# Optimization experiments

Measured on AMD Instinct MI355X. Metric: run time of the kernel, lower is better.

The kernel has to match this reference:

```python
import jax, jax.numpy as jnp
import numpy as np

W0_SIREN = 30.0  # omega_0 used in sine activations

HID = [64, 64, 256, 256, 256]
IN_DIM = 65   # 64 feat channels + 1 time channel
OUT_DIM = 64


def _siren_params(key):
    dims = [IN_DIM] + HID + [OUT_DIM]
    params = []
    for i in range(len(dims) - 1):
        fan_in, fan_out = dims[i], dims[i + 1]
        key, kw, kb = jax.random.split(key, 3)
        if i == 0:
            bound = 1.0 / fan_in
        else:
            bound = np.sqrt(6.0 / fan_in) / W0_SIREN
        W = jax.random.uniform(kw, (fan_out, fan_in), jnp.float32, -bound, bound)
        b = jax.random.uniform(kb, (fan_out,), jnp.float32, -bound, bound)
        params.append((W, b))
    return params


def setup_inputs() -> dict:
    key = jax.random.key(0)
    k_feat, k_t, k_p = jax.random.split(key, 3)
    feat = jax.random.normal(k_feat, (2, 64, 192, 320), jnp.float32)
    times = jax.random.uniform(k_t, (3,), jnp.float32)
    params = _siren_params(k_p)
    inp = {"feat": feat, "times": times}
    for i, (W, b) in enumerate(params):
        inp[f"w{i}"] = W
        inp[f"b{i}"] = b
    return inp


def _gather_full_grid(feat):
    """Nearest grid_sample (align_corners=False) at pixel-center coords over the full grid.
    Returns [B, H*W, C]."""
    B, C, H, W = feat.shape
    # make_coord pixel centers in [-1, 1]
    ys = -1.0 + (2.0 * jnp.arange(H, dtype=jnp.float32) + 1.0) / H
    xs = -1.0 + (2.0 * jnp.arange(W, dtype=jnp.float32) + 1.0) / W
    gy, gx = jnp.meshgrid(ys, xs, indexing="ij")          # [H, W] each
    gy, gx = gy.reshape(-1), gx.reshape(-1)               # [qs]
    # grid_sample nearest, align_corners=False unnormalization
    iy = jnp.clip(jnp.round(((gy + 1.0) * H - 1.0) / 2.0).astype(jnp.int32), 0, H - 1)
    ix = jnp.clip(jnp.round(((gx + 1.0) * W - 1.0) / 2.0).astype(jnp.int32), 0, W - 1)
    q = feat[:, :, iy, ix]                                # [B, C, qs] gather
    return jnp.transpose(q, (0, 2, 1))                    # [B, qs, C]


def _siren_mlp(x, ws, bs):
    h = x
    n = len(ws)
    for i in range(n - 1):
        h = jnp.sin(W0_SIREN * (h @ ws[i].T + bs[i]))
    return h @ ws[n - 1].T + bs[n - 1]                    # outermost linear


def reference(feat, times, w0, b0, w1, b1, w2, b2, w3, b3, w4, b4, w5, b5):
    ws = [w0, w1, w2, w3, w4, w5]
    bs = [b0, b1, b2, b3, b4, b5]
    B, C, H, W = feat.shape
    qs = H * W
    q_feat = _gather_full_grid(feat)                      # [B, qs, 64]
    preds = []
    for c in range(3):  # Training==True branch: 3 time stamps
        t = times[c]
        pe = jnp.full((B, qs, 1), 1.0, feat.dtype) * t    # time channel
        enc = jnp.concatenate([q_feat, pe], axis=-1)      # [B, qs, 65]
        out = _siren_mlp(enc.reshape(B * qs, IN_DIM), ws, bs)  # [B*qs, 64]
        # F.fold with kernel_size=1 == reshape back to spatial map
        pred = out.reshape(B, qs, OUT_DIM).transpose(0, 2, 1).reshape(B, OUT_DIM, H, W)
        preds.append(pred)
    return jnp.stack(preds, axis=0)                       # [3, B, 64, H, W]
```

## Files before the change

### kernel.cpp

```cpp
#include <hip/hip_runtime.h>
#include <hip/hip_bf16.h>

typedef __bf16 bf16_t;
typedef bf16_t bf16x8 __attribute__((ext_vector_type(8)));
typedef float f32x4 __attribute__((ext_vector_type(4)));
typedef unsigned short u16;
typedef unsigned int u32;

static constexpr int kHW = 192 * 320;
static constexpr float kC = 4.77464829275686f;

__device__ __forceinline__ u16 f2bf(float f) {
  u32 u = __float_as_uint(f);
  return (u16)((u + 0x7FFFu + ((u >> 16) & 1u)) >> 16);
}

__device__ __forceinline__ u32 pack2(float a, float b) {
  __hip_bfloat162 h = __float22bfloat162_rn(make_float2(a, b));
  union { __hip_bfloat162 h2; u32 u; } cv;
  cv.h2 = h;
  return cv.u;
}

__device__ __forceinline__ void lds_barrier() {
  __asm__ volatile("s_waitcnt lgkmcnt(0)\n\ts_barrier" ::: "memory");
}

static constexpr int OFF_W0 = 0;
static constexpr int OFF_W1 = 4096;
static constexpr int OFF_W2 = 8192;
static constexpr int OFF_W3 = 24576;
static constexpr int OFF_W4 = 90112;
static constexpr int OFF_W5 = 155648;
static constexpr int W_TOTAL = 172032;
static constexpr int B_TOTAL = 1024;
static constexpr size_t FEAT_BYTE_OFF = 348160;
static constexpr size_t WS_NEED = FEAT_BYTE_OFF + (size_t)1920 * 8192;

__global__ void convert_weights(const float* __restrict__ w0, const float* __restrict__ w1,
                                const float* __restrict__ w2, const float* __restrict__ w3,
                                const float* __restrict__ w4, const float* __restrict__ w5,
                                const float* __restrict__ b0, const float* __restrict__ b1,
                                const float* __restrict__ b2, const float* __restrict__ b3,
                                const float* __restrict__ b4, const float* __restrict__ b5,
                                u16* __restrict__ wb, float* __restrict__ bws) {
  int i = blockIdx.x * 256 + threadIdx.x;
  if (i < W_TOTAL) {
    float v, s = kC;
    if (i < OFF_W1)      { int o = i >> 6, k = i & 63; v = w0[o * 65 + k]; }
    else if (i < OFF_W2) { v = w1[i - OFF_W1]; }
    else if (i < OFF_W3) { v = w2[i - OFF_W2]; }
    else if (i < OFF_W4) { v = w3[i - OFF_W3]; }
    else if (i < OFF_W5) { v = w4[i - OFF_W4]; }
    else                 { v = w5[i - OFF_W5]; s = 1.0f; }
    wb[i] = f2bf(v * s);
  } else {
    int j = i - W_TOTAL;
    float v;
    if (j < 64)       v = kC * b0[j];
    else if (j < 128) v = kC * w0[(j - 64) * 65 + 64];
    else if (j < 192) v = kC * b1[j - 128];
    else if (j < 448) v = kC * b2[j - 192];
    else if (j < 704) v = kC * b3[j - 448];
    else if (j < 960) v = kC * b4[j - 704];
    else              v = b5[j - 960];
    bws[j] = v;
  }
}

__global__ void convert_feat(const float* __restrict__ feat, u16* __restrict__ featT) {
  const int chunk = blockIdx.x;
  const int bq  = chunk / 960;
  const int hw0 = (chunk % 960) * 64;
  const int tid = threadIdx.x;
  const int p   = tid & 63;
  const int gg  = tid >> 6;
  const float* fbase = feat + (size_t)bq * 64 * kHW + hw0 + p;
  u16* img = featT + (size_t)chunk * 4096;
#pragma unroll
  for (int j = 0; j < 2; ++j) {
    const int g = gg * 2 + j;
    float v[8];
#pragma unroll
    for (int e = 0; e < 8; ++e) v[e] = fbase[(size_t)(g * 8 + e) * kHW];
    uint4 pk;
    pk.x = pack2(v[0], v[1]);
    pk.y = pack2(v[2], v[3]);
    pk.z = pack2(v[4], v[5]);
    pk.w = pack2(v[6], v[7]);
    *reinterpret_cast<uint4*>(img + p * 64 + ((g ^ (p & 7)) * 8)) = pk;
  }
}

template<int RSO>
__device__ __forceinline__ void epilogue_sin(f32x4 acc, u16* outb, int p, int g,
                                             int quad, int sw) {
  float s0 = __builtin_amdgcn_sinf(__builtin_amdgcn_fractf(acc[0]));
  float s1 = __builtin_amdgcn_sinf(__builtin_amdgcn_fractf(acc[1]));
  float s2 = __builtin_amdgcn_sinf(__builtin_amdgcn_fractf(acc[2]));
  float s3 = __builtin_amdgcn_sinf(__builtin_amdgcn_fractf(acc[3]));
  uint2 v;
  v.x = pack2(s0, s1);
  v.y = pack2(s2, s3);
  *reinterpret_cast<uint2*>(outb + p * RSO + ((g ^ sw) * 8) + (quad & 1) * 4) = v;
}

__device__ __forceinline__ f32x4 mf(bf16x8 a, bf16x8 b, f32x4 c) {
  return __builtin_amdgcn_mfma_f32_16x16x32_bf16(a, b, c, 0, 0, 0);
}

template<bool PRE>
__global__ __attribute__((amdgpu_waves_per_eu(2, 2)))
void __launch_bounds__(256)
siren_main(const float* __restrict__ feat, const float* __restrict__ times,
           const u16* __restrict__ wb, const float* __restrict__ bws,
           const u16* __restrict__ featT, float* __restrict__ out) {
  __shared__ __align__(16) u16 A32[64 * 256];
  __shared__ __align__(16) u16 B32[64 * 256];
  u16* X = B32;
  u16* Y = B32 + 4096;

  const int tid   = threadIdx.x;
  const int bid   = blockIdx.x;
  const int c     = bid / 1920;
  const int chunk = bid % 1920;
  const int bq    = chunk / 960;
  const int hw0   = (chunk % 960) * 64;
  const float t   = times[c];
  const int wave  = tid >> 6;
  const int lane  = tid & 63;
  const int l15   = lane & 15;
  const int quad  = lane >> 4;
  const int sw    = l15 & 7;

  auto read_af8 = [&](bf16x8 (&af)[8], const u16* in, int pt) {
#pragma unroll
    for (int ks = 0; ks < 8; ++ks)
      af[ks] = *reinterpret_cast<const bf16x8*>(
          in + (pt * 16 + l15) * 256 + (((ks * 4 + quad) ^ sw) * 8));
  };
  auto read_af2 = [&](bf16x8 (&af)[2], const u16* in, int pt) {
#pragma unroll
    for (int ks = 0; ks < 2; ++ks)
      af[ks] = *reinterpret_cast<const bf16x8*>(
          in + (pt * 16 + l15) * 64 + (((ks * 4 + quad) ^ sw) * 8));
  };
  auto load_wf_half = [&](bf16x8 (&wf)[4][4], const u16* wbase, int kh) {
#pragma unroll
    for (int ks = 0; ks < 4; ++ks)
#pragma unroll
      for (int ot = 0; ot < 4; ++ot)
        wf[ot][ks] = *reinterpret_cast<const bf16x8*>(
            wbase + ((wave * 4 + ot) * 16 + l15) * 256 + (kh * 4 + ks) * 32 + quad * 8);
  };
  auto load_bv4 = [&](f32x4 (&bv)[4], const float* bg) {
#pragma unroll
    for (int ot = 0; ot < 4; ++ot)
      bv[ot] = *reinterpret_cast<const f32x4*>(bg + (wave * 4 + ot) * 16 + quad * 4);
  };
  auto mfma_pair = [&](f32x4 (&accA)[4], f32x4 (&accB)[4],
                       bf16x8 (&wa)[4][4], bf16x8 (&wbh)[4][4],
                       bf16x8 (&afA)[8], bf16x8 (&afB)[8], const f32x4 (&bv)[4]) {
#pragma unroll
    for (int ot = 0; ot < 4; ++ot) { accA[ot] = bv[ot]; accB[ot] = bv[ot]; }
#pragma unroll
    for (int ks = 0; ks < 8; ++ks)
#pragma unroll
      for (int ot = 0; ot < 4; ++ot) {
        bf16x8 w = ks < 4 ? wa[ot][ks] : wbh[ot][ks - 4];
        accA[ot] = mf(w, afA[ks], accA[ot]);
        accB[ot] = mf(w, afB[ks], accB[ot]);
      }
  };
  auto epi_pt4 = [&](f32x4 (&acc)[4], u16* outb, int pt) {
#pragma unroll
    for (int ot = 0; ot < 4; ++ot)
      epilogue_sin<256>(acc[ot], outb, pt * 16 + l15,
                        (wave * 4 + ot) * 2 + (quad >> 1), quad, sw);
  };

  bf16x8 wf0[2], wf1[2];
#pragma unroll
  for (int ks = 0; ks < 2; ++ks) {
    wf0[ks] = *reinterpret_cast<const bf16x8*>(wb + OFF_W0 + (wave * 16 + l15) * 64 + ks * 32 + quad * 8);
    wf1[ks] = *reinterpret_cast<const bf16x8*>(wb + OFF_W1 + (wave * 16 + l15) * 64 + ks * 32 + quad * 8);
  }
  f32x4 bv0, bv1;
  {
    f32x4 cb = *reinterpret_cast<const f32x4*>(bws + wave * 16 + quad * 4);
    f32x4 cw = *reinterpret_cast<const f32x4*>(bws + 64 + wave * 16 + quad * 4);
#pragma unroll
    for (int r = 0; r < 4; ++r) bv0[r] = cb[r] + t * cw[r];
    bv1 = *reinterpret_cast<const f32x4*>(bws + 128 + wave * 16 + quad * 4);
  }

  bf16x8 wf2[4][2];
  f32x4  bv2[4];

  if constexpr (PRE) {
    const u16* fsrc = featT + (size_t)chunk * 4096;
    bf16x8 a[4][2];
#pragma unroll
    for (int p = 0; p < 4; ++p)
#pragma unroll
      for (int ks = 0; ks < 2; ++ks)
        a[p][ks] = *reinterpret_cast<const bf16x8*>(
            fsrc + (p * 16 + l15) * 64 + (((ks * 4 + quad) ^ sw) * 8));
#pragma unroll
    for (int ks = 0; ks < 2; ++ks)
#pragma unroll
      for (int ot = 0; ot < 4; ++ot)
        wf2[ot][ks] = *reinterpret_cast<const bf16x8*>(
            wb + OFF_W2 + ((wave * 4 + ot) * 16 + l15) * 64 + ks * 32 + quad * 8);
    load_bv4(bv2, bws + 192);

    f32x4 accp[4];
#pragma unroll
    for (int p = 0; p < 4; ++p) accp[p] = bv0;
#pragma unroll
    for (int ks = 0; ks < 2; ++ks)
#pragma unroll
      for (int p = 0; p < 4; ++p) accp[p] = mf(wf0[ks], a[p][ks], accp[p]);
#pragma unroll
    for (int p = 0; p < 4; ++p)
      epilogue_sin<64>(accp[p], Y, p * 16 + l15, wave * 2 + (quad >> 1), quad, sw);
  } else {
    {
      const int p  = tid & 63;
      const int gg = tid >> 6;
      const float* fbase = feat + (size_t)bq * 64 * kHW + hw0 + p;
#pragma unroll
      for (int j = 0; j < 2; ++j) {
        const int g = gg * 2 + j;
        float v[8];
#pragma unroll
        for (int e = 0; e < 8; ++e) v[e] = fbase[(size_t)(g * 8 + e) * kHW];
        uint4 pk;
        pk.x = pack2(v[0], v[1]);
        pk.y = pack2(v[2], v[3]);
        pk.z = pack2(v[4], v[5]);
        pk.w = pack2(v[6], v[7]);
        *reinterpret_cast<uint4*>(X + p * 64 + ((g ^ (p & 7)) * 8)) = pk;
      }
    }
    lds_barrier();
#pragma unroll
    for (int ks = 0; ks < 2; ++ks)
#pragma unroll
      for (int ot = 0; ot < 4; ++ot)
        wf2[ot][ks] = *reinterpret_cast<const bf16x8*>(
            wb + OFF_W2 + ((wave * 4 + ot) * 16 + l15) * 64 + ks * 32 + quad * 8);
    load_bv4(bv2, bws + 192);
#pragma unroll
    for (int pt = 0; pt < 4; ++pt) {
      bf16x8 a[2];
      read_af2(a, X, pt);
      f32x4 acc = bv0;
      acc = mf(wf0[0], a[0], acc); acc = mf(wf0[1], a[1], acc);
      epilogue_sin<64>(acc, Y, pt * 16 + l15, wave * 2 + (quad >> 1), quad, sw);
    }
  }
  lds_barrier();

  bf16x8 wf3a[4][4], wf3b[4][4];
  f32x4  bv3[4];
  {
    bf16x8 a[4][2];
    read_af2(a[0], Y, 0);
    read_af2(a[1], Y, 1);
    read_af2(a[2], Y, 2);
    read_af2(a[3], Y, 3);
    load_wf_half(wf3a, wb + OFF_W3, 0);
    load_bv4(bv3, bws + 448);
    f32x4 accp[4];
#pragma unroll
    for (int p = 0; p < 4; ++p) accp[p] = bv1;
#pragma unroll
    for (int ks = 0; ks < 2; ++ks)
#pragma unroll
      for (int p = 0; p < 4; ++p) accp[p] = mf(wf1[ks], a[p][ks], accp[p]);
#pragma unroll
    for (int p = 0; p < 4; ++p)
      epilogue_sin<64>(accp[p], X, p * 16 + l15, wave * 2 + (quad >> 1), quad, sw);
  }
  lds_barrier();

  {
    bf16x8 aA[2], aB[2];
    read_af2(aA, X, 0);
    read_af2(aB, X, 1);
    f32x4 accA[4], accB[4];
#pragma unroll
    for (int ot = 0; ot < 4; ++ot) { accA[ot] = bv2[ot]; accB[ot] = bv2[ot]; }
#pragma unroll
    for (int ks = 0; ks < 2; ++ks)
#pragma unroll
      for (int ot = 0; ot < 4; ++ot) {
        accA[ot] = mf(wf2[ot][ks], aA[ks], accA[ot]);
        accB[ot] = mf(wf2[ot][ks], aB[ks], accB[ot]);
      }
    read_af2(aA, X, 2);
    read_af2(aB, X, 3);
    epi_pt4(accA, A32, 0);
    epi_pt4(accB, A32, 1);
#pragma unroll
    for (int ot = 0; ot < 4; ++ot) { accA[ot] = bv2[ot]; accB[ot] = bv2[ot]; }
#pragma unroll
    for (int ks = 0; ks < 2; ++ks)
#pragma unroll
      for (int ot = 0; ot < 4; ++ot) {
        accA[ot] = mf(wf2[ot][ks], aA[ks], accA[ot]);
        accB[ot] = mf(wf2[ot][ks], aB[ks], accB[ot]);
      }
    load_wf_half(wf3b, wb + OFF_W3, 1);
    epi_pt4(accA, A32, 2);
    epi_pt4(accB, A32, 3);
  }
  lds_barrier();

  bf16x8 wf4a[4][4], wf4b[4][4];
  f32x4  bv4[4];
  {
    bf16x8 afA[8], afB[8];
    read_af8(afA, A32, 0);
    read_af8(afB, A32, 1);
    f32x4 accA[4], accB[4];
    mfma_pair(accA, accB, wf3a, wf3b, afA, afB, bv3);
    read_af8(afA, A32, 2);
    read_af8(afB, A32, 3);
    epi_pt4(accA, B32, 0);
    epi_pt4(accB, B32, 1);
    mfma_pair(accA, accB, wf3a, wf3b, afA, afB, bv3);
    load_wf_half(wf4a, wb + OFF_W4, 0);
    load_bv4(bv4, bws + 704);
    epi_pt4(accA, B32, 2);
    epi_pt4(accB, B32, 3);
  }
  lds_barrier();

  bf16x8 wf5[8];
  f32x4  bv5;
  {
    load_wf_half(wf4b, wb + OFF_W4, 1);
    bf16x8 afA[8], afB[8];
    read_af8(afA, B32, 0);
    read_af8(afB, B32, 1);
    f32x4 accA[4], accB[4];
    mfma_pair(accA, accB, wf4a, wf4b, afA, afB, bv4);
    read_af8(afA, B32, 2);
    read_af8(afB, B32, 3);
    epi_pt4(accA, A32, 0);
    epi_pt4(accB, A32, 1);
    mfma_pair(accA, accB, wf4a, wf4b, afA, afB, bv4);
#pragma unroll
    for (int ks = 0; ks < 8; ++ks)
      wf5[ks] = *reinterpret_cast<const bf16x8*>(
          wb + OFF_W5 + (wave * 16 + l15) * 256 + ks * 32 + quad * 8);
    bv5 = *reinterpret_cast<const f32x4*>(bws + 960 + wave * 16 + quad * 4);
    epi_pt4(accA, A32, 2);
    epi_pt4(accB, A32, 3);
  }
  lds_barrier();

  {
    float* out_base = out + (size_t)(c * 2 + bq) * 64 * kHW + hw0;
    const int o = wave * 16 + quad * 4;
    bf16x8 afA[8], afB[8];
    read_af8(afA, A32, 0);
    read_af8(afB, A32, 1);
#pragma unroll
    for (int pp = 0; pp < 2; ++pp) {
      f32x4 accA = bv5, accB = bv5;
#pragma unroll
      for (int ks = 0; ks < 8; ++ks) {
        accA = mf(wf5[ks], afA[ks], accA);
        accB = mf(wf5[ks], afB[ks], accB);
      }
      if (pp == 0) { read_af8(afA, A32, 2); read_af8(afB, A32, 3); }
      const int ptA = pp * 2, ptB = pp * 2 + 1;
      float* dstA = out_base + (size_t)o * kHW + (ptA * 16 + l15);
      float* dstB = out_base + (size_t)o * kHW + (ptB * 16 + l15);
#pragma unroll
      for (int r = 0; r < 4; ++r) dstA[(size_t)r * kHW] = accA[r];
#pragma unroll
      for (int r = 0; r < 4; ++r) dstB[(size_t)r * kHW] = accB[r];
    }
  }
}

extern "C" void kernel_launch(void* const* d_in, const int* in_sizes, int n_in,
                              void* d_out, int out_size, void* d_ws, size_t ws_size,
                              hipStream_t stream) {
  const float* feat  = (const float*)d_in[0];
  const float* times = (const float*)d_in[1];
  const float* w0 = (const float*)d_in[2];
  const float* b0 = (const float*)d_in[3];
  const float* w1 = (const float*)d_in[4];
  const float* b1 = (const float*)d_in[5];
  const float* w2 = (const float*)d_in[6];
  const float* b2 = (const float*)d_in[7];
  const float* w3 = (const float*)d_in[8];
  const float* b3 = (const float*)d_in[9];
  const float* w4 = (const float*)d_in[10];
  const float* b4 = (const float*)d_in[11];
  const float* w5 = (const float*)d_in[12];
  const float* b5 = (const float*)d_in[13];
  u16*   wb  = (u16*)d_ws;
  float* bws = (float*)((char*)d_ws + (size_t)W_TOTAL * 2);
  float* out = (float*)d_out;

  convert_weights<<<(W_TOTAL + B_TOTAL) / 256, 256, 0, stream>>>(
      w0, w1, w2, w3, w4, w5, b0, b1, b2, b3, b4, b5, wb, bws);

  if (ws_size >= WS_NEED) {
    u16* featT = (u16*)((char*)d_ws + FEAT_BYTE_OFF);
    convert_feat<<<1920, 256, 0, stream>>>(feat, featT);
    siren_main<true><<<5760, 256, 0, stream>>>(feat, times, wb, bws, featT, out);
  } else {
    siren_main<false><<<5760, 256, 0, stream>>>(feat, times, wb, bws, wb, out);
  }
}
```

Measured before the change: 386.5 us.

## Double block to 128 points with 8 waves, halving per-wave weight tiles

Each block now handles 128 query points with 512 threads (8 waves) instead of 64 points with 256 threads. In the 256-wide layers each wave owns 32 output channels instead of 64, so the full weight tile for one layer fits in registers at once. The small layers are split by point halves across the two wave groups. The aim is to cut weight-fragment register pressure and amortise weight loads over more points per block. In exchange the block uses twice the LDS (128 KB total), barriers span more waves, and occupancy per CU may change.

```diff
diff --git a/kernel.cpp b/kernel.cpp
--- a/kernel.cpp
+++ b/kernel.cpp
@@ -111,27 +111,29 @@
 
 template<bool PRE>
 __global__ __attribute__((amdgpu_waves_per_eu(2, 2)))
-void __launch_bounds__(256)
+void __launch_bounds__(512)
 siren_main(const float* __restrict__ feat, const float* __restrict__ times,
            const u16* __restrict__ wb, const float* __restrict__ bws,
            const u16* __restrict__ featT, float* __restrict__ out) {
-  __shared__ __align__(16) u16 A32[64 * 256];
-  __shared__ __align__(16) u16 B32[64 * 256];
+  __shared__ __align__(16) u16 A32[128 * 256];
+  __shared__ __align__(16) u16 B32[128 * 256];
   u16* X = B32;
-  u16* Y = B32 + 4096;
+  u16* Y = B32 + 8192;
 
   const int tid   = threadIdx.x;
   const int bid   = blockIdx.x;
-  const int c     = bid / 1920;
-  const int chunk = bid % 1920;
-  const int bq    = chunk / 960;
-  const int hw0   = (chunk % 960) * 64;
+  const int c     = bid / 960;
+  const int pair  = bid % 960;
+  const int bq    = pair / 480;
+  const int hw0   = (pair % 480) * 128;
   const float t   = times[c];
   const int wave  = tid >> 6;
   const int lane  = tid & 63;
   const int l15   = lane & 15;
   const int quad  = lane >> 4;
   const int sw    = l15 & 7;
+  const int wlo   = wave & 3;
+  const int p0    = (wave >> 2) * 4;
 
   auto read_af8 = [&](bf16x8 (&af)[8], const u16* in, int pt) {
 #pragma unroll
@@ -145,89 +147,87 @@
       af[ks] = *reinterpret_cast<const bf16x8*>(
           in + (pt * 16 + l15) * 64 + (((ks * 4 + quad) ^ sw) * 8));
   };
-  auto load_wf_half = [&](bf16x8 (&wf)[4][4], const u16* wbase, int kh) {
-#pragma unroll
-    for (int ks = 0; ks < 4; ++ks)
-#pragma unroll
-      for (int ot = 0; ot < 4; ++ot)
+  auto load_wf16 = [&](bf16x8 (&wf)[2][8], const u16* wbase) {
+#pragma unroll
+    for (int ot = 0; ot < 2; ++ot)
+#pragma unroll
+      for (int ks = 0; ks < 8; ++ks)
         wf[ot][ks] = *reinterpret_cast<const bf16x8*>(
-            wbase + ((wave * 4 + ot) * 16 + l15) * 256 + (kh * 4 + ks) * 32 + quad * 8);
-  };
-  auto load_bv4 = [&](f32x4 (&bv)[4], const float* bg) {
-#pragma unroll
-    for (int ot = 0; ot < 4; ++ot)
-      bv[ot] = *reinterpret_cast<const f32x4*>(bg + (wave * 4 + ot) * 16 + quad * 4);
-  };
-  auto mfma_pair = [&](f32x4 (&accA)[4], f32x4 (&accB)[4],
-                       bf16x8 (&wa)[4][4], bf16x8 (&wbh)[4][4],
-                       bf16x8 (&afA)[8], bf16x8 (&afB)[8], const f32x4 (&bv)[4]) {
-#pragma unroll
-    for (int ot = 0; ot < 4; ++ot) { accA[ot] = bv[ot]; accB[ot] = bv[ot]; }
+            wbase + ((wave * 2 + ot) * 16 + l15) * 256 + ks * 32 + quad * 8);
+  };
+  auto load_bv2 = [&](f32x4 (&bv)[2], const float* bg) {
+#pragma unroll
+    for (int ot = 0; ot < 2; ++ot)
+      bv[ot] = *reinterpret_cast<const f32x4*>(bg + (wave * 2 + ot) * 16 + quad * 4);
+  };
+  auto mfma_pair2 = [&](f32x4 (&accA)[2], f32x4 (&accB)[2], bf16x8 (&wf)[2][8],
+                        bf16x8 (&afA)[8], bf16x8 (&afB)[8], const f32x4 (&bv)[2]) {
+#pragma unroll
+    for (int ot = 0; ot < 2; ++ot) { accA[ot] = bv[ot]; accB[ot] = bv[ot]; }
 #pragma unroll
     for (int ks = 0; ks < 8; ++ks)
 #pragma unroll
-      for (int ot = 0; ot < 4; ++ot) {
-        bf16x8 w = ks < 4 ? wa[ot][ks] : wbh[ot][ks - 4];
-        accA[ot] = mf(w, afA[ks], accA[ot]);
-        accB[ot] = mf(w, afB[ks], accB[ot]);
+      for (int ot = 0; ot < 2; ++ot) {
+        accA[ot] = mf(wf[ot][ks], afA[ks], accA[ot]);
+        accB[ot] = mf(wf[ot][ks], afB[ks], accB[ot]);
       }
   };
-  auto epi_pt4 = [&](f32x4 (&acc)[4], u16* outb, int pt) {
-#pragma unroll
-    for (int ot = 0; ot < 4; ++ot)
+  auto epi_pt2 = [&](f32x4 (&acc)[2], u16* outb, int pt) {
+#pragma unroll
+    for (int ot = 0; ot < 2; ++ot)
       epilogue_sin<256>(acc[ot], outb, pt * 16 + l15,
-                        (wave * 4 + ot) * 2 + (quad >> 1), quad, sw);
+                        (wave * 2 + ot) * 2 + (quad >> 1), quad, sw);
   };
 
   bf16x8 wf0[2], wf1[2];
 #pragma unroll
   for (int ks = 0; ks < 2; ++ks) {
-    wf0[ks] = *reinterpret_cast<const bf16x8*>(wb + OFF_W0 + (wave * 16 + l15) * 64 + ks * 32 + quad * 8);
-    wf1[ks] = *reinterpret_cast<const bf16x8*>(wb + OFF_W1 + (wave * 16 + l15) * 64 + ks * 32 + quad * 8);
+    wf0[ks] = *reinterpret_cast<const bf16x8*>(wb + OFF_W0 + (wlo * 16 + l15) * 64 + ks * 32 + quad * 8);
+    wf1[ks] = *reinterpret_cast<const bf16x8*>(wb + OFF_W1 + (wlo * 16 + l15) * 64 + ks * 32 + quad * 8);
   }
   f32x4 bv0, bv1;
   {
-    f32x4 cb = *reinterpret_cast<const f32x4*>(bws + wave * 16 + quad * 4);
-    f32x4 cw = *reinterpret_cast<const f32x4*>(bws + 64 + wave * 16 + quad * 4);
+    f32x4 cb = *reinterpret_cast<const f32x4*>(bws + wlo * 16 + quad * 4);
+    f32x4 cw = *reinterpret_cast<const f32x4*>(bws + 64 + wlo * 16 + quad * 4);
 #pragma unroll
     for (int r = 0; r < 4; ++r) bv0[r] = cb[r] + t * cw[r];
-    bv1 = *reinterpret_cast<const f32x4*>(bws + 128 + wave * 16 + quad * 4);
-  }
-
-  bf16x8 wf2[4][2];
-  f32x4  bv2[4];
+    bv1 = *reinterpret_cast<const f32x4*>(bws + 128 + wlo * 16 + quad * 4);
+  }
+
+  bf16x8 wf2[2][2];
+  f32x4  bv2[2];
 
   if constexpr (PRE) {
-    const u16* fsrc = featT + (size_t)chunk * 4096;
+    const u16* fsrc = featT + (size_t)pair * 8192;
     bf16x8 a[4][2];
 #pragma unroll
     for (int p = 0; p < 4; ++p)
 #pragma unroll
       for (int ks = 0; ks < 2; ++ks)
         a[p][ks] = *reinterpret_cast<const bf16x8*>(
-            fsrc + (p * 16 + l15) * 64 + (((ks * 4 + quad) ^ sw) * 8));
+            fsrc + ((p0 + p) * 16 + l15) * 64 + (((ks * 4 + quad) ^ sw) * 8));
+#pragma unroll
+    for (int ot = 0; ot < 2; ++ot)
+#pragma unroll
+      for (int ks = 0; ks < 2; ++ks)
+        wf2[ot][ks] = *reinterpret_cast<const bf16x8*>(
+            wb + OFF_W2 + ((wave * 2 + ot) * 16 + l15) * 64 + ks * 32 + quad * 8);
+    load_bv2(bv2, bws + 192);
+
+    f32x4 accp[4];
+#pragma unroll
+    for (int p = 0; p < 4; ++p) accp[p] = bv0;
 #pragma unroll
     for (int ks = 0; ks < 2; ++ks)
 #pragma unroll
-      for (int ot = 0; ot < 4; ++ot)
-        wf2[ot][ks] = *reinterpret_cast<const bf16x8*>(
-            wb + OFF_W2 + ((wave * 4 + ot) * 16 + l15) * 64 + ks * 32 + quad * 8);
-    load_bv4(bv2, bws + 192);
-
-    f32x4 accp[4];
-#pragma unroll
-    for (int p = 0; p < 4; ++p) accp[p] = bv0;
-#pragma unroll
-    for (int ks = 0; ks < 2; ++ks)
-#pragma unroll
       for (int p = 0; p < 4; ++p) accp[p] = mf(wf0[ks], a[p][ks], accp[p]);
 #pragma unroll
     for (int p = 0; p < 4; ++p)
-      epilogue_sin<64>(accp[p], Y, p * 16 + l15, wave * 2 + (quad >> 1), quad, sw);
+      epilogue_sin<64>(accp[p], Y, (p0 + p) * 16 + l15, wlo * 2 + (quad >> 1), quad, sw);
   } else {
     {
-      const int p  = tid & 63;
-      const int gg = tid >> 6;
+      const int p  = tid & 127;
+      const int gg = tid >> 7;
       const float* fbase = feat + (size_t)bq * 64 * kHW + hw0 + p;
 #pragma unroll
       for (int j = 0; j < 2; ++j) {
@@ -245,33 +245,33 @@
     }
     lds_barrier();
 #pragma unroll
-    for (int ks = 0; ks < 2; ++ks)
-#pragma unroll
-      for (int ot = 0; ot < 4; ++ot)
+    for (int ot = 0; ot < 2; ++ot)
+#pragma unroll
+      for (int ks = 0; ks < 2; ++ks)
         wf2[ot][ks] = *reinterpret_cast<const bf16x8*>(
-            wb + OFF_W2 + ((wave * 4 + ot) * 16 + l15) * 64 + ks * 32 + quad * 8);
-    load_bv4(bv2, bws + 192);
-#pragma unroll
-    for (int pt = 0; pt < 4; ++pt) {
+            wb + OFF_W2 + ((wave * 2 + ot) * 16 + l15) * 64 + ks * 32 + quad * 8);
+    load_bv2(bv2, bws + 192);
+#pragma unroll
+    for (int p = 0; p < 4; ++p) {
       bf16x8 a[2];
-      read_af2(a, X, pt);
+      read_af2(a, X, p0 + p);
       f32x4 acc = bv0;
       acc = mf(wf0[0], a[0], acc); acc = mf(wf0[1], a[1], acc);
-      epilogue_sin<64>(acc, Y, pt * 16 + l15, wave * 2 + (quad >> 1), quad, sw);
+      epilogue_sin<64>(acc, Y, (p0 + p) * 16 + l15, wlo * 2 + (quad >> 1), quad, sw);
     }
   }
   lds_barrier();
 
-  bf16x8 wf3a[4][4], wf3b[4][4];
-  f32x4  bv3[4];
+  bf16x8 wf3[2][8];
+  f32x4  bv3[2];
   {
     bf16x8 a[4][2];
-    read_af2(a[0], Y, 0);
-    read_af2(a[1], Y, 1);
-    read_af2(a[2], Y, 2);
-    read_af2(a[3], Y, 3);
-    load_wf_half(wf3a, wb + OFF_W3, 0);
-    load_bv4(bv3, bws + 448);
+    read_af2(a[0], Y, p0);
+    read_af2(a[1], Y, p0 + 1);
+    read_af2(a[2], Y, p0 + 2);
+    read_af2(a[3], Y, p0 + 3);
+    load_wf16(wf3, wb + OFF_W3);
+    load_bv2(bv3, bws + 448);
     f32x4 accp[4];
 #pragma unroll
     for (int p = 0; p < 4; ++p) accp[p] = bv1;
@@ -281,7 +281,7 @@
       for (int p = 0; p < 4; ++p) accp[p] = mf(wf1[ks], a[p][ks], accp[p]);
 #pragma unroll
     for (int p = 0; p < 4; ++p)
-      epilogue_sin<64>(accp[p], X, p * 16 + l15, wave * 2 + (quad >> 1), quad, sw);
+      epilogue_sin<64>(accp[p], X, (p0 + p) * 16 + l15, wlo * 2 + (quad >> 1), quad, sw);
   }
   lds_barrier();
 
@@ -289,85 +289,99 @@
     bf16x8 aA[2], aB[2];
     read_af2(aA, X, 0);
     read_af2(aB, X, 1);
-    f32x4 accA[4], accB[4];
-#pragma unroll
-    for (int ot = 0; ot < 4; ++ot) { accA[ot] = bv2[ot]; accB[ot] = bv2[ot]; }
-#pragma unroll
-    for (int ks = 0; ks < 2; ++ks)
-#pragma unroll
-      for (int ot = 0; ot < 4; ++ot) {
-        accA[ot] = mf(wf2[ot][ks], aA[ks], accA[ot]);
-        accB[ot] = mf(wf2[ot][ks], aB[ks], accB[ot]);
+    f32x4 accA[2], accB[2];
+#pragma unroll
+    for (int pp = 0; pp < 4; ++pp) {
+#pragma unroll
+      for (int ot = 0; ot < 2; ++ot) { accA[ot] = bv2[ot]; accB[ot] = bv2[ot]; }
+#pragma unroll
+      for (int ks = 0; ks < 2; ++ks)
+#pragma unroll
+        for (int ot = 0; ot < 2; ++ot) {
+          accA[ot] = mf(wf2[ot][ks], aA[ks], accA[ot]);
+          accB[ot] = mf(wf2[ot][ks], aB[ks], accB[ot]);
+        }
+      if (pp < 3) {
+        read_af2(aA, X, pp * 2 + 2);
+        read_af2(aB, X, pp * 2 + 3);
       }
-    read_af2(aA, X, 2);
-    read_af2(aB, X, 3);
-    epi_pt4(accA, A32, 0);
-    epi_pt4(accB, A32, 1);
-#pragma unroll
-    for (int ot = 0; ot < 4; ++ot) { accA[ot] = bv2[ot]; accB[ot] = bv2[ot]; }
-#pragma unroll
-    for (int ks = 0; ks < 2; ++ks)
-#pragma unroll
-      for (int ot = 0; ot < 4; ++ot) {
-        accA[ot] = mf(wf2[ot][ks], aA[ks], accA[ot]);
-        accB[ot] = mf(wf2[ot][ks], aB[ks], accB[ot]);
-      }
-    load_wf_half(wf3b, wb + OFF_W3, 1);
-    epi_pt4(accA, A32, 2);
-    epi_pt4(accB, A32, 3);
+      epi_pt2(accA, A32, pp * 2);
+      epi_pt2(accB, A32, pp * 2 + 1);
+    }
   }
   lds_barrier();
 
-  bf16x8 wf4a[4][4], wf4b[4][4];
-  f32x4  bv4[4];
+  bf16x8 wf4[2][8];
+  f32x4  bv4[2];
   {
     bf16x8 afA[8], afB[8];
+    f32x4 accA[2], accB[2];
     read_af8(afA, A32, 0);
     read_af8(afB, A32, 1);
-    f32x4 accA[4], accB[4];
-    mfma_pair(accA, accB, wf3a, wf3b, afA, afB, bv3);
+    mfma_pair2(accA, accB, wf3, afA, afB, bv3);
     read_af8(afA, A32, 2);
     read_af8(afB, A32, 3);
-    epi_pt4(accA, B32, 0);
-    epi_pt4(accB, B32, 1);
-    mfma_pair(accA, accB, wf3a, wf3b, afA, afB, bv3);
-    load_wf_half(wf4a, wb + OFF_W4, 0);
-    load_bv4(bv4, bws + 704);
-    epi_pt4(accA, B32, 2);
-    epi_pt4(accB, B32, 3);
+    epi_pt2(accA, B32, 0);
+    epi_pt2(accB, B32, 1);
+    mfma_pair2(accA, accB, wf3, afA, afB, bv3);
+    read_af8(afA, A32, 4);
+    read_af8(afB, A32, 5);
+    __builtin_amdgcn_sched_barrier(0);
+    load_wf16(wf4, wb + OFF_W4);
+    load_bv2(bv4, bws + 704);
+    epi_pt2(accA, B32, 2);
+    epi_pt2(accB, B32, 3);
+    mfma_pair2(accA, accB, wf3, afA, afB, bv3);
+    read_af8(afA, A32, 6);
+    read_af8(afB, A32, 7);
+    epi_pt2(accA, B32, 4);
+    epi_pt2(accB, B32, 5);
+    mfma_pair2(accA, accB, wf3, afA, afB, bv3);
+    epi_pt2(accA, B32, 6);
+    epi_pt2(accB, B32, 7);
   }
   lds_barrier();
 
   bf16x8 wf5[8];
   f32x4  bv5;
   {
-    load_wf_half(wf4b, wb + OFF_W4, 1);
     bf16x8 afA[8], afB[8];
+    f32x4 accA[2], accB[2];
     read_af8(afA, B32, 0);
     read_af8(afB, B32, 1);
-    f32x4 accA[4], accB[4];
-    mfma_pair(accA, accB, wf4a, wf4b, afA, afB, bv4);
+    mfma_pair2(accA, accB, wf4, afA, afB, bv4);
     read_af8(afA, B32, 2);
     read_af8(afB, B32, 3);
-    epi_pt4(accA, A32, 0);
-    epi_pt4(accB, A32, 1);
-    mfma_pair(accA, accB, wf4a, wf4b, afA, afB, bv4);
+    epi_pt2(accA, A32, 0);
+    epi_pt2(accB, A32, 1);
+    mfma_pair2(accA, accB, wf4, afA, afB, bv4);
+    read_af8(afA, B32, 4);
+    read_af8(afB, B32, 5);
+    __builtin_amdgcn_sched_barrier(0);
 #pragma unroll
     for (int ks = 0; ks < 8; ++ks)
       wf5[ks] = *reinterpret_cast<const bf16x8*>(
-          wb + OFF_W5 + (wave * 16 + l15) * 256 + ks * 32 + quad * 8);
-    bv5 = *reinterpret_cast<const f32x4*>(bws + 960 + wave * 16 + quad * 4);
-    epi_pt4(accA, A32, 2);
-    epi_pt4(accB, A32, 3);
+          wb + OFF_W5 + (wlo * 16 + l15) * 256 + ks * 32 + quad * 8);
+    bv5 = *reinterpret_cast<const f32x4*>(bws + 960 + wlo * 16 + quad * 4);
+    epi_pt2(accA, A32, 2);
+    epi_pt2(accB, A32, 3);
+    mfma_pair2(accA, accB, wf4, afA, afB, bv4);
+    read_af8(afA, B32, 6);
+    read_af8(afB, B32, 7);
+    epi_pt2(accA, A32, 4);
+    epi_pt2(accB, A32, 5);
+    mfma_pair2(accA, accB, wf4, afA, afB, bv4);
+    epi_pt2(accA, A32, 6);
+    epi_pt2(accB, A32, 7);
   }
   lds_barrier();
 
   {
     float* out_base = out + (size_t)(c * 2 + bq) * 64 * kHW + hw0;
-    const int o = wave * 16 + quad * 4;
+    const int o = wlo * 16 + quad * 4;
     bf16x8 afA[8], afB[8];
-    read_af8(afA, A32, 0);
-    read_af8(afB, A32, 1);
+    read_af8(afA, A32, p0);
+    read_af8(afB, A32, p0 + 1);
 #pragma unroll
     for (int pp = 0; pp < 2; ++pp) {
       f32x4 accA = bv5, accB = bv5;
@@ -376,8 +390,8 @@
         accA = mf(wf5[ks], afA[ks], accA);
         accB = mf(wf5[ks], afB[ks], accB);
       }
-      if (pp == 0) { read_af8(afA, A32, 2); read_af8(afB, A32, 3); }
-      const int ptA = pp * 2, ptB = pp * 2 + 1;
+      if (pp == 0) { read_af8(afA, A32, p0 + 2); read_af8(afB, A32, p0 + 3); }
+      const int ptA = p0 + pp * 2, ptB = p0 + pp * 2 + 1;
       float* dstA = out_base + (size_t)o * kHW + (ptA * 16 + l15);
       float* dstB = out_base + (size_t)o * kHW + (ptB * 16 + l15);
 #pragma unroll
@@ -415,8 +429,8 @@
   if (ws_size >= WS_NEED) {
     u16* featT = (u16*)((char*)d_ws + FEAT_BYTE_OFF);
     convert_feat<<<1920, 256, 0, stream>>>(feat, featT);
-    siren_main<true><<<5760, 256, 0, stream>>>(feat, times, wb, bws, featT, out);
+    siren_main<true><<<2880, 512, 0, stream>>>(feat, times, wb, bws, featT, out);
   } else {
-    siren_main<false><<<5760, 256, 0, stream>>>(feat, times, wb, bws, wb, out);
-  }
-}
+    siren_main<false><<<2880, 512, 0, stream>>>(feat, times, wb, bws, wb, out);
+  }
+}
```

Result: faster. 336.8 us, median of 2 (-12.9%).
